# Performance work log

Hardware: AMD Instinct MI355X
Metric: run time of the kernel (lower is better)

## Reference

```python
import jax, jax.numpy as jnp
import numpy as np

N_NODES = 100000
N_EDGES = 1600000
DIMS = [(2, 128), (128, 128), (128, 32), (32, 32), (32, 32)]


def setup_inputs() -> dict:
    key = jax.random.key(0)
    ks = jax.random.split(key, 2 + 3 * len(DIMS) + 2)
    x = jax.random.normal(ks[0], (N_NODES, 2), dtype=jnp.float32)
    edge_index = jax.random.randint(ks[1], (2, N_EDGES), 0, N_NODES, dtype=jnp.int32)
    inp = {"x": x, "edge_index": edge_index, "batch_size": 100}
    k = 2
    for i, (cin, cout) in enumerate(DIMS, start=1):
        s = 1.0 / np.sqrt(cin)
        inp[f"Wl{i}"] = jax.random.normal(ks[k], (cin, cout), dtype=jnp.float32) * s; k += 1
        inp[f"bl{i}"] = jnp.zeros((cout,), dtype=jnp.float32)
        inp[f"Wr{i}"] = jax.random.normal(ks[k], (cin, cout), dtype=jnp.float32) * s; k += 1
    inp["W_out"] = jax.random.normal(ks[k], (32, 1), dtype=jnp.float32) * (1.0 / np.sqrt(32.0)); k += 1
    inp["b_out"] = jnp.zeros((1,), dtype=jnp.float32)
    return inp


def reference(x, edge_index, batch_size,
              Wl1, bl1, Wr1, Wl2, bl2, Wr2, Wl3, bl3, Wr3,
              Wl4, bl4, Wr4, Wl5, bl5, Wr5, W_out, b_out):
    src, dst = edge_index[0], edge_index[1]
    h = x.reshape(-1, 2)
    n = h.shape[0]
    # in-degree per target node, clamped to 1 (PyG mean aggr gives 0 for isolated nodes)
    deg = jax.ops.segment_sum(jnp.ones_like(src, dtype=h.dtype), dst, num_segments=n)
    inv_deg = (1.0 / jnp.maximum(deg, 1.0))[:, None]

    def sage(h, Wl, bl, Wr):
        # mean-aggregate neighbor features, then SAGEConv: lin_l(agg) + lin_r(h)
        agg = jax.ops.segment_sum(h[src], dst, num_segments=n) * inv_deg
        return agg @ Wl + bl + h @ Wr

    for Wl, bl, Wr in ((Wl1, bl1, Wr1), (Wl2, bl2, Wr2), (Wl3, bl3, Wr3),
                       (Wl4, bl4, Wr4), (Wl5, bl5, Wr5)):
        h = jax.nn.relu(sage(h, Wl, bl, Wr))
    # dropout is identity in eval mode
    out = h @ W_out + b_out  # [n, 1]
    return out.reshape(batch_size, -1)
```

## Files before the change

### kernel.cpp

```cpp
#include <hip/hip_runtime.h>
#include <hip/hip_bf16.h>

#define N_NODES 100000
#define N_EDGES 1600000
#define NBUCK 256
#define NODES_PER_BUCKET 391
#define EDGES_PER_CHUNK (N_EDGES / NBUCK)
#define FILL_LDS_CAP 8192

typedef __bf16 bf16x8 __attribute__((ext_vector_type(8)));
typedef float f32x4 __attribute__((ext_vector_type(4)));


__device__ inline unsigned short f2bf_rne(float v) {
    unsigned u = __float_as_uint(v);
    u += 0x7fffu + ((u >> 16) & 1u);
    return (unsigned short)(u >> 16);
}

__device__ inline unsigned pack_bf(float a, float b) {
    return (unsigned)f2bf_rne(a) | ((unsigned)f2bf_rne(b) << 16);
}

__device__ inline void acc8_bf(float* a, uint4 p) {
    a[0] += __uint_as_float(p.x << 16);
    a[1] += __uint_as_float(p.x & 0xffff0000u);
    a[2] += __uint_as_float(p.y << 16);
    a[3] += __uint_as_float(p.y & 0xffff0000u);
    a[4] += __uint_as_float(p.z << 16);
    a[5] += __uint_as_float(p.z & 0xffff0000u);
    a[6] += __uint_as_float(p.w << 16);
    a[7] += __uint_as_float(p.w & 0xffff0000u);
}


__global__ __launch_bounds__(256) void pa_count(const int* __restrict__ dst,
                                                int* __restrict__ blkCntT) {
    __shared__ int hist[NBUCK];
    hist[threadIdx.x] = 0;
    __syncthreads();
    int b0 = blockIdx.x * EDGES_PER_CHUNK;
    int b1 = min(b0 + EDGES_PER_CHUNK, N_EDGES);
    for (int i = b0 + (int)threadIdx.x; i < b1; i += 256) {
        int d = __builtin_nontemporal_load(&dst[i]);
        atomicAdd(&hist[d / NODES_PER_BUCKET], 1);
    }
    __syncthreads();
    blkCntT[threadIdx.x * NBUCK + blockIdx.x] = hist[threadIdx.x];
}

__global__ __launch_bounds__(256) void pa_scan1(const int* __restrict__ blkCntT,
                                                int* __restrict__ blkBaseL,
                                                int* __restrict__ bucketTotal) {
    __shared__ int s[256];
    int t = threadIdx.x;
    int v = blkCntT[blockIdx.x * NBUCK + t];
    s[t] = v;
    __syncthreads();
    for (int off = 1; off < 256; off <<= 1) {
        int u = (t >= off) ? s[t - off] : 0;
        __syncthreads();
        s[t] += u;
        __syncthreads();
    }
    blkBaseL[blockIdx.x * NBUCK + t] = s[t] - v;
    if (t == 255) bucketTotal[blockIdx.x] = s[255];
}

__global__ __launch_bounds__(256) void pa_scan2(const int* __restrict__ bucketTotal,
                                                int* __restrict__ bstart,
                                                int* __restrict__ offsets) {
    __shared__ int s[256];
    int t = threadIdx.x;
    int v = bucketTotal[t];
    s[t] = v;
    __syncthreads();
    for (int off = 1; off < 256; off <<= 1) {
        int u = (t >= off) ? s[t - off] : 0;
        __syncthreads();
        s[t] += u;
        __syncthreads();
    }
    bstart[t] = s[t] - v;
    if (t == 255) {
        bstart[256] = s[255];
        offsets[N_NODES] = s[255];
    }
}

__global__ __launch_bounds__(256) void pa_scatter(const int* __restrict__ src,
                                                  const int* __restrict__ dst,
                                                  const int* __restrict__ blkCntT,
                                                  const int* __restrict__ blkBaseL,
                                                  const int* __restrict__ bstart,
                                                  int2* __restrict__ staging) {
    __shared__ int runStart[NBUCK];
    __shared__ int cur[NBUCK];
    __shared__ int gbase[NBUCK];
    __shared__ int2 buf[EDGES_PER_CHUNK];

    const int tid = threadIdx.x;
    const int g = blockIdx.x;
    const int b0 = g * EDGES_PER_CHUNK;
    const int b1 = min(b0 + EDGES_PER_CHUNK, N_EDGES);

    {
        __shared__ int s[256];
        int v = blkCntT[tid * NBUCK + g];
        s[tid] = v;
        __syncthreads();
        for (int off = 1; off < 256; off <<= 1) {
            int u = (tid >= off) ? s[tid - off] : 0;
            __syncthreads();
            s[tid] += u;
            __syncthreads();
        }
        runStart[tid] = s[tid] - v;
        cur[tid] = s[tid] - v;
        gbase[tid] = bstart[tid] + blkBaseL[tid * NBUCK + g];
    }
    __syncthreads();
    for (int i = b0 + tid; i < b1; i += 256) {
        int d = __builtin_nontemporal_load(&dst[i]);
        int s_ = __builtin_nontemporal_load(&src[i]);
        int k = d / NODES_PER_BUCKET;
        int p = atomicAdd(&cur[k], 1);
        buf[p] = make_int2(s_, d);
    }
    __syncthreads();
    int cnt = b1 - b0;
    for (int i = tid; i < cnt; i += 256) {
        int2 e = buf[i];
        int k = e.y / NODES_PER_BUCKET;
        staging[gbase[k] + (i - runStart[k])] = e;
    }
}

__global__ __launch_bounds__(512) void pc_fill(const int2* __restrict__ staging,
                                               const int* __restrict__ bstart,
                                               int* __restrict__ ssrc,
                                               int* __restrict__ offsets,
                                               float* __restrict__ inv_deg) {
    __shared__ int scnt[NODES_PER_BUCKET];
    __shared__ int sexc[NODES_PER_BUCKET];
    __shared__ int scur[NODES_PER_BUCKET];
    __shared__ int ssrcL[FILL_LDS_CAP];

    const int tid = threadIdx.x;
    const int b = blockIdx.x;
    const int node0 = b * NODES_PER_BUCKET;
    const int nn = min(node0 + NODES_PER_BUCKET, N_NODES) - node0;
    if (nn <= 0) return;
    const int es = bstart[b], ee = bstart[b + 1];
    const int cnt = ee - es;

    for (int j = tid; j < nn; j += 512) scnt[j] = 0;
    __syncthreads();
    for (int i = es + tid; i < ee; i += 512) {
        int2 e = staging[i];
        atomicAdd(&scnt[e.y - node0], 1);
    }
    __syncthreads();

    if (tid < 64) {
        int base = tid * 7;
        int vals[7];
        int run = 0;
#pragma unroll
        for (int j = 0; j < 7; ++j) {
            int idx = base + j;
            int c = (idx < nn) ? scnt[idx] : 0;
            vals[j] = run;
            run += c;
        }
        int inc = run;
#pragma unroll
        for (int off = 1; off < 64; off <<= 1) {
            int u = __shfl_up(inc, off, 64);
            if (tid >= off) inc += u;
        }
        int laneExcl = inc - run;
#pragma unroll
        for (int j = 0; j < 7; ++j) {
            int idx = base + j;
            if (idx < nn) sexc[idx] = laneExcl + vals[j];
        }
    }
    __syncthreads();

    for (int j = tid; j < nn; j += 512) {
        int c = scnt[j];
        int ex = sexc[j];
        offsets[node0 + j] = es + ex;
        inv_deg[node0 + j] = 1.0f / (float)max(c, 1);
        scur[j] = ex;
    }
    __syncthreads();

    if (cnt <= FILL_LDS_CAP) {
        for (int i = es + tid; i < ee; i += 512) {
            int2 e = staging[i];
            int p = atomicAdd(&scur[e.y - node0], 1);
            ssrcL[p] = e.x;
        }
        __syncthreads();
        for (int i = tid; i < cnt; i += 512) ssrc[es + i] = ssrcL[i];
    } else {
        for (int i = es + tid; i < ee; i += 512) {
            int2 e = staging[i];
            int p = atomicAdd(&scur[e.y - node0], 1);
            ssrc[es + p] = e.x;
        }
    }
}


__global__ __launch_bounds__(256) void sage1_fused(const float* __restrict__ x,
                                                   const int* __restrict__ offs,
                                                   const int* __restrict__ ssrc,
                                                   const float* __restrict__ inv_deg,
                                                   const float* __restrict__ Wl,
                                                   const float* __restrict__ bl,
                                                   const float* __restrict__ Wr,
                                                   unsigned short* __restrict__ out_bf,
                                                   int nnodes) {
    int t = blockIdx.x * 256 + threadIdx.x;
    int node = t >> 2;
    int c = t & 3;
    if (node >= nnodes) return;
    const float2* __restrict__ x2 = (const float2*)x;
    int b = offs[node], e = offs[node + 1];
    float ax = 0.f, ay = 0.f;
    for (int i = b + c; i < e; i += 4) {
        float2 v = x2[ssrc[i]];
        ax += v.x;
        ay += v.y;
    }
    ax += __shfl_xor(ax, 1, 4);
    ay += __shfl_xor(ay, 1, 4);
    ax += __shfl_xor(ax, 2, 4);
    ay += __shfl_xor(ay, 2, 4);
    float s = inv_deg[node];
    ax *= s; ay *= s;
    float2 hh = x2[node];
    const float* wl0 = Wl + c * 32;
    const float* wl1 = Wl + 128 + c * 32;
    const float* wr0 = Wr + c * 32;
    const float* wr1 = Wr + 128 + c * 32;
    const float* bb = bl + c * 32;
    uint4* dst4 = (uint4*)(out_bf + (size_t)node * 128 + c * 32);
#pragma unroll
    for (int q = 0; q < 4; ++q) {
        unsigned vals[4];
#pragma unroll
        for (int pj = 0; pj < 4; ++pj) {
            int j = q * 8 + pj * 2;
            float v0 = fmaxf(bb[j] + ax * wl0[j] + ay * wl1[j] +
                             hh.x * wr0[j] + hh.y * wr1[j], 0.f);
            float v1 = fmaxf(bb[j + 1] + ax * wl0[j + 1] + ay * wl1[j + 1] +
                             hh.x * wr0[j + 1] + hh.y * wr1[j + 1], 0.f);
            vals[pj] = pack_bf(v0, v1);
        }
        dst4[q] = make_uint4(vals[0], vals[1], vals[2], vals[3]);
    }
}


__global__ __launch_bounds__(256) void aggregate_bf128(const unsigned short* __restrict__ hb,
                                                       const int* __restrict__ offs,
                                                       const int* __restrict__ ssrc,
                                                       const float* __restrict__ inv_deg,
                                                       unsigned short* __restrict__ aggb,
                                                       int nnodes) {
    int t = blockIdx.x * 256 + threadIdx.x;
    if (t >= nnodes * 16) return;
    int node = t >> 4;
    int c = t & 15;
    int b = offs[node], e = offs[node + 1];
    const uint4* __restrict__ hb4 = (const uint4*)hb;
    float acc[8] = {0.f, 0.f, 0.f, 0.f, 0.f, 0.f, 0.f, 0.f};
    int i = b;
    for (; i + 4 <= e; i += 4) {
        uint4 p0 = hb4[(size_t)ssrc[i] * 16 + c];
        uint4 p1 = hb4[(size_t)ssrc[i + 1] * 16 + c];
        uint4 p2 = hb4[(size_t)ssrc[i + 2] * 16 + c];
        uint4 p3 = hb4[(size_t)ssrc[i + 3] * 16 + c];
        acc8_bf(acc, p0);
        acc8_bf(acc, p1);
        acc8_bf(acc, p2);
        acc8_bf(acc, p3);
    }
    for (; i < e; ++i) {
        uint4 p = hb4[(size_t)ssrc[i] * 16 + c];
        acc8_bf(acc, p);
    }
    float s = inv_deg[node];
    uint4 o;
    o.x = pack_bf(acc[0] * s, acc[1] * s);
    o.y = pack_bf(acc[2] * s, acc[3] * s);
    o.z = pack_bf(acc[4] * s, acc[5] * s);
    o.w = pack_bf(acc[6] * s, acc[7] * s);
    ((uint4*)aggb)[t] = o;
}


__global__ __launch_bounds__(256) void prep_all(const float* __restrict__ Wl2,
                                                const float* __restrict__ Wr2,
                                                const float* __restrict__ Wl3,
                                                const float* __restrict__ Wr3,
                                                const float* __restrict__ Wl4,
                                                const float* __restrict__ Wr4,
                                                const float* __restrict__ Wl5,
                                                const float* __restrict__ Wr5,
                                                unsigned short* __restrict__ Wt,
                                                unsigned short* __restrict__ W3c,
                                                unsigned short* __restrict__ W4c,
                                                unsigned short* __restrict__ W5c) {
    int idx = blockIdx.x * 256 + threadIdx.x;
    if (idx < 32768) {
        int n = idx >> 8, k = idx & 255;
        float v = (k < 128) ? Wl2[k * 128 + n] : Wr2[(k - 128) * 128 + n];
        Wt[idx] = f2bf_rne(v);
    } else if (idx < 32768 + 8192) {
        int j = idx - 32768;
        int n = j >> 7, k = j & 127;
        float v = (n < 32) ? Wl3[k * 32 + n] : Wr3[k * 32 + (n - 32)];
        W3c[j] = f2bf_rne(v);
    } else if (idx < 32768 + 8192 + 2048) {
        int j = idx - 32768 - 8192;
        int n = j >> 5, k = j & 31;
        float v = (n < 32) ? Wl4[k * 32 + n] : Wr4[k * 32 + (n - 32)];
        W4c[j] = f2bf_rne(v);
    } else if (idx < 32768 + 8192 + 4096) {
        int j = idx - 32768 - 8192 - 2048;
        int n = j >> 5, k = j & 31;
        float v = (n < 32) ? Wl5[k * 32 + n] : Wr5[k * 32 + (n - 32)];
        W5c[j] = f2bf_rne(v);
    }
}


__global__ __launch_bounds__(256) void gemm_l2_mfma(const unsigned short* __restrict__ Ab,
                                                    const unsigned short* __restrict__ Hb,
                                                    const unsigned short* __restrict__ Wt,
                                                    const float* __restrict__ bias,
                                                    const unsigned short* __restrict__ W3c,
                                                    unsigned short* __restrict__ g3b,
                                                    float* __restrict__ p3, int M) {
    constexpr int BM = 128, BK = 64;
    __shared__ unsigned short smem[26112];
#define SA(r, c) smem[(r) * 72 + (c)]
#define SB(r, c) smem[9216 + (r) * 72 + (c)]
#define SH(r, c) smem[(r) * 136 + (c)]
#define SW3(r, c) smem[17408 + (r) * 136 + (c)]

    const int tid = threadIdx.x;
    const int m0 = blockIdx.x * BM;
    const int lane = tid & 63;
    const int wid = tid >> 6;
    const int l15 = lane & 15;
    const int quad = lane >> 4;
    const int wm = (wid >> 1) * 64;
    const int wn = (wid & 1) * 64;

    f32x4 acc[4][4];
#pragma unroll
    for (int i = 0; i < 4; ++i)
#pragma unroll
        for (int j = 0; j < 4; ++j) acc[i][j] = (f32x4){0.f, 0.f, 0.f, 0.f};

    for (int k0 = 0; k0 < 256; k0 += BK) {
        const uint4* __restrict__ srcA = (const uint4*)((k0 < 128) ? Ab : Hb);
        const int kc = (k0 & 64) >> 3;
#pragma unroll
        for (int l = 0; l < 4; ++l) {
            int idx = tid + l * 256;
            int row = idx >> 3;
            int c8 = idx & 7;
            int gr = min(m0 + row, M - 1);
            uint4 va = srcA[(size_t)gr * 16 + kc + c8];
            *(uint4*)&SA(row, c8 * 8) = va;
            uint4 vb = ((const uint4*)Wt)[(size_t)row * 32 + (k0 >> 3) + c8];
            *(uint4*)&SB(row, c8 * 8) = vb;
        }
        __syncthreads();

#pragma unroll
        for (int ks = 0; ks < BK; ks += 32) {
            bf16x8 a[4], b[4];
#pragma unroll
            for (int t = 0; t < 4; ++t) {
                a[t] = *(const bf16x8*)&SA(wm + t * 16 + l15, ks + quad * 8);
                b[t] = *(const bf16x8*)&SB(wn + t * 16 + l15, ks + quad * 8);
            }
#pragma unroll
            for (int i = 0; i < 4; ++i)
#pragma unroll
                for (int j = 0; j < 4; ++j)
                    acc[i][j] = __builtin_amdgcn_mfma_f32_16x16x32_bf16(
                        a[i], b[j], acc[i][j], 0, 0, 0);
        }
        __syncthreads();
    }

#pragma unroll
    for (int j = 0; j < 4; ++j) {
        int n = wn + j * 16 + l15;
        float bv = bias[n];
#pragma unroll
        for (int i = 0; i < 4; ++i) {
#pragma unroll
            for (int r = 0; r < 4; ++r) {
                int ml = wm + i * 16 + quad * 4 + r;
                SH(ml, n) = f2bf_rne(fmaxf(acc[i][j][r] + bv, 0.f));
            }
        }
    }
#pragma unroll
    for (int l = 0; l < 4; ++l) {
        int idx = tid + l * 256;
        int row = idx >> 4;
        int c8 = idx & 15;
        uint4 v = ((const uint4*)W3c)[(size_t)row * 16 + c8];
        *(uint4*)&SW3(row, c8 * 8) = v;
    }
    __syncthreads();

    f32x4 acc2[2][4];
#pragma unroll
    for (int i = 0; i < 2; ++i)
#pragma unroll
        for (int j = 0; j < 4; ++j) acc2[i][j] = (f32x4){0.f, 0.f, 0.f, 0.f};

#pragma unroll
    for (int ks = 0; ks < 128; ks += 32) {
        bf16x8 a[2], b[4];
#pragma unroll
        for (int i = 0; i < 2; ++i)
            a[i] = *(const bf16x8*)&SH(wid * 32 + i * 16 + l15, ks + quad * 8);
#pragma unroll
        for (int j = 0; j < 4; ++j)
            b[j] = *(const bf16x8*)&SW3(j * 16 + l15, ks + quad * 8);
#pragma unroll
        for (int i = 0; i < 2; ++i)
#pragma unroll
            for (int j = 0; j < 4; ++j)
                acc2[i][j] = __builtin_amdgcn_mfma_f32_16x16x32_bf16(
                    a[i], b[j], acc2[i][j], 0, 0, 0);
    }

#pragma unroll
    for (int i = 0; i < 2; ++i) {
#pragma unroll
        for (int r = 0; r < 4; ++r) {
            int m = m0 + wid * 32 + i * 16 + quad * 4 + r;
            if (m >= M) continue;
#pragma unroll
            for (int j = 0; j < 4; ++j) {
                float v = acc2[i][j][r];
                if (j < 2) g3b[(size_t)m * 32 + j * 16 + l15] = f2bf_rne(v);
                else       p3[(size_t)m * 32 + (j - 2) * 16 + l15] = v;
            }
        }
    }
#undef SA
#undef SB
#undef SH
#undef SW3
}


__global__ __launch_bounds__(256) void aggregate_combine32(
        const unsigned short* __restrict__ gb_prev,
        const int* __restrict__ offs,
        const int* __restrict__ ssrc,
        const float* __restrict__ inv_deg,
        const float* __restrict__ p,
        const float* __restrict__ bias,
        const unsigned short* __restrict__ Wc,
        unsigned short* __restrict__ g_next,
        float* __restrict__ p_next, int nnodes) {
    __shared__ unsigned short hB[64][40];
    __shared__ unsigned short wB[64][40];

    const int tid = threadIdx.x;
    const int node0 = blockIdx.x * 64;
    const int node = node0 + (tid >> 2);
    const int c = tid & 3;
    const int ln = tid >> 2;

#pragma unroll
    for (int l = 0; l < 2; ++l) {
        int id = tid + l * 256;
        int r = id >> 3, cc = id & 7;
        uint2 v = ((const uint2*)Wc)[(size_t)r * 8 + cc];
        *(uint2*)&wB[r][cc * 4] = v;
    }

    uint4 hout = make_uint4(0u, 0u, 0u, 0u);
    if (node < nnodes) {
        int b = offs[node], e = offs[node + 1];
        const uint4* __restrict__ hb4 = (const uint4*)gb_prev;
        float acc[8] = {0.f, 0.f, 0.f, 0.f, 0.f, 0.f, 0.f, 0.f};
        int i = b;
        for (; i + 4 <= e; i += 4) {
            uint4 p0 = hb4[(size_t)ssrc[i] * 4 + c];
            uint4 p1 = hb4[(size_t)ssrc[i + 1] * 4 + c];
            uint4 p2 = hb4[(size_t)ssrc[i + 2] * 4 + c];
            uint4 p3 = hb4[(size_t)ssrc[i + 3] * 4 + c];
            acc8_bf(acc, p0);
            acc8_bf(acc, p1);
            acc8_bf(acc, p2);
            acc8_bf(acc, p3);
        }
        for (; i < e; ++i) acc8_bf(acc, hb4[(size_t)ssrc[i] * 4 + c]);
        float s = inv_deg[node];
        const float4* prow = (const float4*)(p + (size_t)node * 32 + c * 8);
        float4 p0 = prow[0], p1 = prow[1];
        const float* bb = bias + c * 8;
        float h0 = fmaxf(acc[0] * s + p0.x + bb[0], 0.f);
        float h1 = fmaxf(acc[1] * s + p0.y + bb[1], 0.f);
        float h2 = fmaxf(acc[2] * s + p0.z + bb[2], 0.f);
        float h3 = fmaxf(acc[3] * s + p0.w + bb[3], 0.f);
        float h4 = fmaxf(acc[4] * s + p1.x + bb[4], 0.f);
        float h5 = fmaxf(acc[5] * s + p1.y + bb[5], 0.f);
        float h6 = fmaxf(acc[6] * s + p1.z + bb[6], 0.f);
        float h7 = fmaxf(acc[7] * s + p1.w + bb[7], 0.f);
        hout.x = pack_bf(h0, h1);
        hout.y = pack_bf(h2, h3);
        hout.z = pack_bf(h4, h5);
        hout.w = pack_bf(h6, h7);
    }
    *(uint4*)&hB[ln][c * 8] = hout;
    __syncthreads();

    const int lane = tid & 63;
    const int wid = tid >> 6;
    const int l15 = lane & 15;
    const int quad = lane >> 4;

    bf16x8 a = *(const bf16x8*)&hB[wid * 16 + l15][quad * 8];
    f32x4 accm[4];
#pragma unroll
    for (int j = 0; j < 4; ++j) {
        bf16x8 b = *(const bf16x8*)&wB[j * 16 + l15][quad * 8];
        accm[j] = __builtin_amdgcn_mfma_f32_16x16x32_bf16(
            a, b, (f32x4){0.f, 0.f, 0.f, 0.f}, 0, 0, 0);
    }

#pragma unroll
    for (int r = 0; r < 4; ++r) {
        int m = node0 + wid * 16 + quad * 4 + r;
        if (m >= nnodes) continue;
#pragma unroll
        for (int j = 0; j < 4; ++j) {
            float v = accm[j][r];
            if (j < 2) g_next[(size_t)m * 32 + j * 16 + l15] = f2bf_rne(v);
            else       p_next[(size_t)m * 32 + (j - 2) * 16 + l15] = v;
        }
    }
}

__global__ __launch_bounds__(256) void aggregate_final32(
        const unsigned short* __restrict__ gb_prev,
        const int* __restrict__ offs,
        const int* __restrict__ ssrc,
        const float* __restrict__ inv_deg,
        const float* __restrict__ p,
        const float* __restrict__ bias,
        const float* __restrict__ Wout,
        const float* __restrict__ bout,
        float* __restrict__ out, int nnodes) {
    int t = blockIdx.x * 256 + threadIdx.x;
    int node = t >> 2;
    int c = t & 3;
    if (node >= nnodes) return;
    int b = offs[node], e = offs[node + 1];
    const uint4* __restrict__ hb4 = (const uint4*)gb_prev;
    float acc[8] = {0.f, 0.f, 0.f, 0.f, 0.f, 0.f, 0.f, 0.f};
    int i = b;
    for (; i + 4 <= e; i += 4) {
        uint4 p0 = hb4[(size_t)ssrc[i] * 4 + c];
        uint4 p1 = hb4[(size_t)ssrc[i + 1] * 4 + c];
        uint4 p2 = hb4[(size_t)ssrc[i + 2] * 4 + c];
        uint4 p3 = hb4[(size_t)ssrc[i + 3] * 4 + c];
        acc8_bf(acc, p0);
        acc8_bf(acc, p1);
        acc8_bf(acc, p2);
        acc8_bf(acc, p3);
    }
    for (; i < e; ++i) acc8_bf(acc, hb4[(size_t)ssrc[i] * 4 + c]);
    float s = inv_deg[node];
    const float4* prow = (const float4*)(p + (size_t)node * 32 + c * 8);
    float4 p0 = prow[0], p1 = prow[1];
    const float* bb = bias + c * 8;
    const float* w = Wout + c * 8;
    float sum = 0.f;
    sum = fmaf(fmaxf(acc[0] * s + p0.x + bb[0], 0.f), w[0], sum);
    sum = fmaf(fmaxf(acc[1] * s + p0.y + bb[1], 0.f), w[1], sum);
    sum = fmaf(fmaxf(acc[2] * s + p0.z + bb[2], 0.f), w[2], sum);
    sum = fmaf(fmaxf(acc[3] * s + p0.w + bb[3], 0.f), w[3], sum);
    sum = fmaf(fmaxf(acc[4] * s + p1.x + bb[4], 0.f), w[4], sum);
    sum = fmaf(fmaxf(acc[5] * s + p1.y + bb[5], 0.f), w[5], sum);
    sum = fmaf(fmaxf(acc[6] * s + p1.z + bb[6], 0.f), w[6], sum);
    sum = fmaf(fmaxf(acc[7] * s + p1.w + bb[7], 0.f), w[7], sum);
    sum += __shfl_down(sum, 2, 4);
    sum += __shfl_down(sum, 1, 4);
    if (c == 0) out[node] = sum + bout[0];
}


extern "C" void kernel_launch(void* const* d_in, const int* in_sizes, int n_in,
                              void* d_out, int out_size, void* d_ws, size_t ws_size,
                              hipStream_t stream) {
    const float* x      = (const float*)d_in[0];
    const int*   ei     = (const int*)d_in[1];
    const float* Wl1    = (const float*)d_in[3];
    const float* bl1    = (const float*)d_in[4];
    const float* Wr1    = (const float*)d_in[5];
    const float* Wl2    = (const float*)d_in[6];
    const float* bl2    = (const float*)d_in[7];
    const float* Wr2    = (const float*)d_in[8];
    const float* Wl3    = (const float*)d_in[9];
    const float* bl3    = (const float*)d_in[10];
    const float* Wr3    = (const float*)d_in[11];
    const float* Wl4    = (const float*)d_in[12];
    const float* bl4    = (const float*)d_in[13];
    const float* Wr4    = (const float*)d_in[14];
    const float* Wl5    = (const float*)d_in[15];
    const float* bl5    = (const float*)d_in[16];
    const float* Wr5    = (const float*)d_in[17];
    const float* W_out  = (const float*)d_in[18];
    const float* b_out  = (const float*)d_in[19];
    float* out = (float*)d_out;

    const int N = N_NODES, E = N_EDGES;
    const int* e_src = ei;
    const int* e_dst = ei + E;

    size_t off = 0;
    auto carve = [&](size_t bytes) {
        void* p = (char*)d_ws + off;
        off += (bytes + 255) & ~(size_t)255;
        return p;
    };
    int*   offsets  = (int*)carve((size_t)(N + 1) * 4);
    float* inv_deg  = (float*)carve((size_t)N * 4);
    int*   ssrc     = (int*)carve((size_t)E * 4);
    int*   blkCntT  = (int*)carve((size_t)NBUCK * NBUCK * 4);
    int*   blkBaseL = (int*)carve((size_t)NBUCK * NBUCK * 4);
    int*   bucketTotal = (int*)carve((size_t)NBUCK * 4);
    int*   bstart   = (int*)carve((size_t)(NBUCK + 1) * 4);
    int2*  staging  = (int2*)carve((size_t)E * 8);
    unsigned short* Wt  = (unsigned short*)carve((size_t)128 * 256 * 2);
    unsigned short* W3c = (unsigned short*)carve((size_t)64 * 128 * 2);
    unsigned short* W4c = (unsigned short*)carve((size_t)64 * 32 * 2);
    unsigned short* W5c = (unsigned short*)carve((size_t)64 * 32 * 2);
    float* agg      = (float*)carve((size_t)N * 128 * 4);
    float* bufA     = (float*)carve((size_t)N * 128 * 4);
    unsigned short* g3b = (unsigned short*)carve((size_t)N * 32 * 2);
    unsigned short* g4b = (unsigned short*)carve((size_t)N * 32 * 2);
    unsigned short* g5b = (unsigned short*)carve((size_t)N * 32 * 2);

    float* slotA = agg;
    float* slotC = agg + (size_t)N * 64;
    unsigned short* h1_bf = (unsigned short*)bufA;
    unsigned short* aggB  = (unsigned short*)bufA + (size_t)N * 128;

    pa_count<<<NBUCK, 256, 0, stream>>>(e_dst, blkCntT);
    pa_scan1<<<NBUCK, 256, 0, stream>>>(blkCntT, blkBaseL, bucketTotal);
    pa_scan2<<<1, 256, 0, stream>>>(bucketTotal, bstart, offsets);
    pa_scatter<<<NBUCK, 256, 0, stream>>>(e_src, e_dst, blkCntT, blkBaseL, bstart, staging);
    pc_fill<<<NBUCK, 512, 0, stream>>>(staging, bstart, ssrc, offsets, inv_deg);
    prep_all<<<176, 256, 0, stream>>>(Wl2, Wr2, Wl3, Wr3, Wl4, Wr4, Wl5, Wr5,
                                      Wt, W3c, W4c, W5c);

    const int gemm_grid = (N + 127) / 128;
    const int comb_grid = (N + 63) / 64;

    sage1_fused<<<(N * 4 + 255) / 256, 256, 0, stream>>>(x, offsets, ssrc, inv_deg,
                                                         Wl1, bl1, Wr1, h1_bf, N);

    aggregate_bf128<<<(N * 16 + 255) / 256, 256, 0, stream>>>(h1_bf, offsets, ssrc,
                                                              inv_deg, aggB, N);
    gemm_l2_mfma<<<gemm_grid, 256, 0, stream>>>(aggB, h1_bf, Wt, bl2, W3c, g3b, slotA, N);

    aggregate_combine32<<<comb_grid, 256, 0, stream>>>(g3b, offsets, ssrc, inv_deg,
                                                       slotA, bl3, W4c, g4b, slotC, N);

    aggregate_combine32<<<comb_grid, 256, 0, stream>>>(g4b, offsets, ssrc, inv_deg,
                                                       slotC, bl4, W5c, g5b, slotA, N);

    aggregate_final32<<<(N * 4 + 255) / 256, 256, 0, stream>>>(g5b, offsets, ssrc, inv_deg,
                                                               slotA, bl5, W_out, b_out,
                                                               out, N);
}
```

Before: 348.2 us.

## Pack staged edges into one int and cache layer-1 weights in LDS

Edges in the bucket staging buffer are now packed as a single 32-bit word holding the source shifted left by 9 bits and the local destination offset, which halves staging traffic in both the scatter and fill kernels. The scatter kernel works out each slot's bucket from the run boundaries in a small byte table instead of dividing again. The fill kernel loads its bucket's edges into LDS once and reuses them for counting and placement. sage1_fused stages Wl, Wr and bl into shared memory rather than reading them from global memory. The packing relies on source indices fitting in 23 bits, which holds for 100000 nodes, and the extra LDS may lower occupancy of pc_fill.

```diff
diff --git a/kernel.cpp b/kernel.cpp
--- a/kernel.cpp
+++ b/kernel.cpp
@@ -93,16 +93,18 @@
                                                   const int* __restrict__ blkCntT,
                                                   const int* __restrict__ blkBaseL,
                                                   const int* __restrict__ bstart,
-                                                  int2* __restrict__ staging) {
-    __shared__ int runStart[NBUCK];
+                                                  int* __restrict__ staging) {
+    __shared__ int runStart[NBUCK + 1];
     __shared__ int cur[NBUCK];
     __shared__ int gbase[NBUCK];
-    __shared__ int2 buf[EDGES_PER_CHUNK];
+    __shared__ int buf[EDGES_PER_CHUNK];
+    __shared__ unsigned char bucketOf[EDGES_PER_CHUNK];
 
     const int tid = threadIdx.x;
     const int g = blockIdx.x;
     const int b0 = g * EDGES_PER_CHUNK;
     const int b1 = min(b0 + EDGES_PER_CHUNK, N_EDGES);
+    const int cnt = b1 - b0;
 
     {
         __shared__ int s[256];
@@ -118,25 +120,28 @@
         runStart[tid] = s[tid] - v;
         cur[tid] = s[tid] - v;
         gbase[tid] = bstart[tid] + blkBaseL[tid * NBUCK + g];
+        if (tid == 255) runStart[256] = s[255];
     }
     __syncthreads();
     for (int i = b0 + tid; i < b1; i += 256) {
         int d = __builtin_nontemporal_load(&dst[i]);
         int s_ = __builtin_nontemporal_load(&src[i]);
         int k = d / NODES_PER_BUCKET;
+        int ld = d - k * NODES_PER_BUCKET;
         int p = atomicAdd(&cur[k], 1);
-        buf[p] = make_int2(s_, d);
-    }
-    __syncthreads();
-    int cnt = b1 - b0;
+        buf[p] = (s_ << 9) | ld;
+    }
+    __syncthreads();
+    for (int i = runStart[tid]; i < runStart[tid + 1]; ++i)
+        bucketOf[i] = (unsigned char)tid;
+    __syncthreads();
     for (int i = tid; i < cnt; i += 256) {
-        int2 e = buf[i];
-        int k = e.y / NODES_PER_BUCKET;
-        staging[gbase[k] + (i - runStart[k])] = e;
-    }
-}
-
-__global__ __launch_bounds__(512) void pc_fill(const int2* __restrict__ staging,
+        int k = bucketOf[i];
+        staging[gbase[k] + (i - runStart[k])] = buf[i];
+    }
+}
+
+__global__ __launch_bounds__(512) void pc_fill(const int* __restrict__ staging,
                                                const int* __restrict__ bstart,
                                                int* __restrict__ ssrc,
                                                int* __restrict__ offsets,
@@ -144,6 +149,7 @@
     __shared__ int scnt[NODES_PER_BUCKET];
     __shared__ int sexc[NODES_PER_BUCKET];
     __shared__ int scur[NODES_PER_BUCKET];
+    __shared__ int ebuf[FILL_LDS_CAP];
     __shared__ int ssrcL[FILL_LDS_CAP];
 
     const int tid = threadIdx.x;
@@ -153,12 +159,18 @@
     if (nn <= 0) return;
     const int es = bstart[b], ee = bstart[b + 1];
     const int cnt = ee - es;
+    const bool inLds = (cnt <= FILL_LDS_CAP);
 
     for (int j = tid; j < nn; j += 512) scnt[j] = 0;
-    __syncthreads();
-    for (int i = es + tid; i < ee; i += 512) {
-        int2 e = staging[i];
-        atomicAdd(&scnt[e.y - node0], 1);
+    if (inLds)
+        for (int i = tid; i < cnt; i += 512) ebuf[i] = staging[es + i];
+    __syncthreads();
+
+    if (inLds) {
+        for (int i = tid; i < cnt; i += 512) atomicAdd(&scnt[ebuf[i] & 511], 1);
+    } else {
+        for (int i = es + tid; i < ee; i += 512)
+            atomicAdd(&scnt[staging[i] & 511], 1);
     }
     __syncthreads();
 
@@ -197,19 +209,19 @@
     }
     __syncthreads();
 
-    if (cnt <= FILL_LDS_CAP) {
-        for (int i = es + tid; i < ee; i += 512) {
-            int2 e = staging[i];
-            int p = atomicAdd(&scur[e.y - node0], 1);
-            ssrcL[p] = e.x;
+    if (inLds) {
+        for (int i = tid; i < cnt; i += 512) {
+            int e = ebuf[i];
+            int p = atomicAdd(&scur[e & 511], 1);
+            ssrcL[p] = e >> 9;
         }
         __syncthreads();
         for (int i = tid; i < cnt; i += 512) ssrc[es + i] = ssrcL[i];
     } else {
         for (int i = es + tid; i < ee; i += 512) {
-            int2 e = staging[i];
-            int p = atomicAdd(&scur[e.y - node0], 1);
-            ssrc[es + p] = e.x;
+            int e = staging[i];
+            int p = atomicAdd(&scur[e & 511], 1);
+            ssrc[es + p] = e >> 9;
         }
     }
 }
@@ -224,7 +236,16 @@
                                                    const float* __restrict__ Wr,
                                                    unsigned short* __restrict__ out_bf,
                                                    int nnodes) {
-    int t = blockIdx.x * 256 + threadIdx.x;
+    __shared__ float wls[256], wrs[256], bls[128];
+    int tid = threadIdx.x;
+    if (tid < 256) {
+        wls[tid] = Wl[tid];
+        wrs[tid] = Wr[tid];
+        if (tid < 128) bls[tid] = bl[tid];
+    }
+    __syncthreads();
+
+    int t = blockIdx.x * 256 + tid;
     int node = t >> 2;
     int c = t & 3;
     if (node >= nnodes) return;
@@ -243,11 +264,11 @@
     float s = inv_deg[node];
     ax *= s; ay *= s;
     float2 hh = x2[node];
-    const float* wl0 = Wl + c * 32;
-    const float* wl1 = Wl + 128 + c * 32;
-    const float* wr0 = Wr + c * 32;
-    const float* wr1 = Wr + 128 + c * 32;
-    const float* bb = bl + c * 32;
+    const float* wl0 = wls + c * 32;
+    const float* wl1 = wls + 128 + c * 32;
+    const float* wr0 = wrs + c * 32;
+    const float* wr1 = wrs + 128 + c * 32;
+    const float* bb = bls + c * 32;
     uint4* dst4 = (uint4*)(out_bf + (size_t)node * 128 + c * 32);
 #pragma unroll
     for (int q = 0; q < 4; ++q) {
@@ -651,7 +672,7 @@
     int*   blkBaseL = (int*)carve((size_t)NBUCK * NBUCK * 4);
     int*   bucketTotal = (int*)carve((size_t)NBUCK * 4);
     int*   bstart   = (int*)carve((size_t)(NBUCK + 1) * 4);
-    int2*  staging  = (int2*)carve((size_t)E * 8);
+    int*   staging  = (int*)carve((size_t)E * 4);
     unsigned short* Wt  = (unsigned short*)carve((size_t)128 * 256 * 2);
     unsigned short* W3c = (unsigned short*)carve((size_t)64 * 128 * 2);
     unsigned short* W4c = (unsigned short*)carve((size_t)64 * 32 * 2);
```

Result: faster. 323.9 us (-7.0%).
